# Optimization experiments

Measured on AMD Instinct MI355X. Metric: run time of the kernel, lower is better.

Reference implementation:

```python
import jax, jax.numpy as jnp
import numpy as np

D_MODEL = 1024
N_HEADS = 16
D_K = D_MODEL // N_HEADS
SCALE = float(np.sqrt(D_K))


def setup_inputs() -> dict:
    key = jax.random.key(0)
    ks = jax.random.split(key, 8)
    B, S = 2, 2048
    init = 1.0 / np.sqrt(D_MODEL)
    return {
        "query": jax.random.normal(ks[0], (B, S, D_MODEL), dtype=jnp.float32),
        "key": jax.random.normal(ks[1], (B, S, D_MODEL), dtype=jnp.float32),
        "value": jax.random.normal(ks[2], (B, S, D_MODEL), dtype=jnp.float32),
        "w_q": jax.random.uniform(ks[3], (D_MODEL, D_MODEL), jnp.float32, -init, init),
        "w_k": jax.random.uniform(ks[4], (D_MODEL, D_MODEL), jnp.float32, -init, init),
        "w_v": jax.random.uniform(ks[5], (D_MODEL, D_MODEL), jnp.float32, -init, init),
        "w_o": jax.random.uniform(ks[6], (D_MODEL, D_MODEL), jnp.float32, -init, init),
        "b_o": jax.random.uniform(ks[7], (D_MODEL,), jnp.float32, -init, init),
    }


def reference(query, key, value, w_q, w_k, w_v, w_o, b_o):
    B, S, _ = query.shape
    # nn.Linear computes x @ W.T; weights stored torch-style [out, in]
    def proj(x, w):
        # [B,S,D] -> [B,H,S,Dk]
        return (x @ w.T).reshape(B, S, N_HEADS, D_K).transpose(0, 2, 1, 3)

    Q = proj(query, w_q)
    K = proj(key, w_k)
    V = proj(value, w_v)
    scores = jnp.einsum("bhqd,bhkd->bhqk", Q, K) / SCALE  # [B,H,S,S]
    attn = jax.nn.softmax(scores, axis=-1)
    out = jnp.einsum("bhqk,bhkd->bhqd", attn, V)  # [B,H,S,Dk]
    out = out.transpose(0, 2, 1, 3).reshape(B, S, D_MODEL)
    out = out @ w_o.T + b_o
    return (out, attn)
```

## Files before the change

kernel.cpp:

```cpp
#include <hip/hip_runtime.h>
#include <hip/hip_bf16.h>

typedef unsigned int u32;
typedef unsigned short u16;
using bf16x8 = __attribute__((ext_vector_type(8))) short;
using f32x4  = __attribute__((ext_vector_type(4))) float;

#define S_LEN 2048
#define DK 64
#define NH 16
#define DMODEL 1024
#define NROWS 4096

__device__ __forceinline__ u16 f2bf(float f){
  u32 u = __builtin_bit_cast(u32, f);
  u += 0x7fffu + ((u >> 16) & 1u);
  return (u16)(u >> 16);
}

__device__ __forceinline__ void gload_lds16(const u16* g, u16* l){
  __builtin_amdgcn_global_load_lds(
      (__attribute__((address_space(1))) u32*)(void*)const_cast<u16*>(g),
      (__attribute__((address_space(3))) u32*)(void*)l, 16, 0, 0);
}

#define BARRIER_VM(N) do { \
  asm volatile("s_waitcnt vmcnt(" #N ") lgkmcnt(0)" ::: "memory"); \
  __builtin_amdgcn_s_barrier(); \
  __builtin_amdgcn_sched_barrier(0); \
} while (0)

__global__ void cvt_all(const float* __restrict__ q, const float* __restrict__ k,
                        const float* __restrict__ v, const float* __restrict__ wq,
                        const float* __restrict__ wk, const float* __restrict__ wv,
                        const float* __restrict__ wo, u16* __restrict__ ws)
{
  const int y = blockIdx.y;
  const int n4 = (y < 3) ? (NROWS*DMODEL/4) : (DMODEL*DMODEL/4);
  const int i = blockIdx.x * blockDim.x + threadIdx.x;
  if (i >= n4) return;
  const float* src = (y==0)?q:(y==1)?k:(y==2)?v:(y==3)?wq:(y==4)?wk:(y==5)?wv:wo;
  u16* dst = ws + ((y < 3) ? (size_t)y*(NROWS*DMODEL)
                           : (size_t)3*(NROWS*DMODEL) + (size_t)(y-3)*(DMODEL*DMODEL));
  float4 val = reinterpret_cast<const float4*>(src)[i];
  ushort4 o;
  o.x = f2bf(val.x); o.y = f2bf(val.y); o.z = f2bf(val.z); o.w = f2bf(val.w);
  reinterpret_cast<ushort4*>(dst)[i] = o;
}

template<bool OUTGEMM>
__global__ __launch_bounds__(256)
void gemm_mha(const u16* __restrict__ Abase, const u16* __restrict__ Bbase,
              u16* __restrict__ Qh, u16* __restrict__ Kh, u16* __restrict__ Vt,
              float* __restrict__ Out, const float* __restrict__ bias)
{
  __shared__ u16 smem[32768];
  u16* As = smem;
  u16* Bs = smem + 16384;

  const int tid  = threadIdx.x;
  const int lane = tid & 63;
  const int wid  = tid >> 6;
  const int lo = lane & 15, hi = lane >> 4;
  const int z = OUTGEMM ? 0 : blockIdx.z;
  const int m0 = blockIdx.x * 128;
  const int n0 = blockIdx.y * 128;
  const u16* ga = Abase + (size_t)z * (NROWS*DMODEL)  + (size_t)m0 * DMODEL;
  const u16* gb = Bbase + (size_t)z * (DMODEL*DMODEL) + (size_t)n0 * DMODEL;

  const int wm = (wid >> 1) * 64;
  const int wn = (wid & 1) * 64;

  f32x4 acc[4][4] = {};

  auto stage = [&](int buf, int kt){
    const u16* a = ga + kt * 64;
    const u16* b = gb + kt * 64;
    #pragma unroll
    for (int i = 0; i < 4; ++i){
      const int chunk = i*256 + tid;
      const int row = chunk >> 3, c8 = chunk & 7;
      gload_lds16(a + (size_t)row*DMODEL + c8*8, &As[buf*8192 + (i*256 + wid*64)*8]);
      gload_lds16(b + (size_t)row*DMODEL + c8*8, &Bs[buf*8192 + (i*256 + wid*64)*8]);
    }
  };

  stage(0, 0);
  __syncthreads();

  for (int t = 0; t < DMODEL/64; ++t){
    const int buf = t & 1;
    if (t + 1 < DMODEL/64) stage(buf ^ 1, t + 1);
    const u16* as = &As[buf*8192];
    const u16* bs = &Bs[buf*8192];
    #pragma unroll
    for (int ks = 0; ks < 2; ++ks){
      bf16x8 af[4], bfr[4];
      #pragma unroll
      for (int i = 0; i < 4; ++i){
        af[i]  = *reinterpret_cast<const bf16x8*>(&as[(wm + i*16 + lo)*64 + ks*32 + hi*8]);
        bfr[i] = *reinterpret_cast<const bf16x8*>(&bs[(wn + i*16 + lo)*64 + ks*32 + hi*8]);
      }
      #pragma unroll
      for (int mi = 0; mi < 4; ++mi)
        #pragma unroll
        for (int ni = 0; ni < 4; ++ni)
          acc[mi][ni] = __builtin_amdgcn_mfma_f32_16x16x32_bf16(af[mi], bfr[ni], acc[mi][ni], 0, 0, 0);
    }
    __syncthreads();
  }

  if constexpr (OUTGEMM){
    #pragma unroll
    for (int mi = 0; mi < 4; ++mi)
    #pragma unroll
    for (int ni = 0; ni < 4; ++ni)
    #pragma unroll
    for (int r = 0; r < 4; ++r){
      const int m = m0 + wm + mi*16 + hi*4 + r;
      const int n = n0 + wn + ni*16 + lo;
      __builtin_nontemporal_store(acc[mi][ni][r] + bias[n],
                                  &Out[(size_t)m * DMODEL + n]);
    }
  } else {
    const float scale = (z == 0) ? 0.18033688011112043f : 1.0f;
    if (z == 2){
      #pragma unroll
      for (int mi = 0; mi < 4; ++mi)
      #pragma unroll
      for (int ni = 0; ni < 4; ++ni)
      #pragma unroll
      for (int r = 0; r < 4; ++r)
        smem[(size_t)(wn + ni*16 + lo)*136 + wm + mi*16 + hi*4 + r] = f2bf(acc[mi][ni][r]);
    } else {
      #pragma unroll
      for (int mi = 0; mi < 4; ++mi)
      #pragma unroll
      for (int ni = 0; ni < 4; ++ni)
      #pragma unroll
      for (int r = 0; r < 4; ++r)
        smem[(size_t)(wm + mi*16 + hi*4 + r)*136 + wn + ni*16 + lo] = f2bf(acc[mi][ni][r] * scale);
    }
    __syncthreads();
    const int b = m0 >> 11, s0 = m0 & 2047;
    #pragma unroll
    for (int it = 0; it < 8; ++it){
      const int c = it*256 + tid;
      const int rr = c >> 4, cc = c & 15;
      bf16x8 v = *reinterpret_cast<const bf16x8*>(&smem[(size_t)rr*136 + cc*8]);
      if (z == 2){
        const int gn = n0 + rr, h = gn >> 6, d = gn & 63;
        *reinterpret_cast<bf16x8*>(&Vt[(((size_t)(b*NH + h))*DK + d)*S_LEN + s0 + cc*8]) = v;
      } else {
        const int gn = n0 + cc*8, h = gn >> 6, d0 = gn & 63;
        u16* dst = z ? Kh : Qh;
        *reinterpret_cast<bf16x8*>(&dst[(((size_t)(b*NH + h))*S_LEN + s0 + rr)*DK + d0]) = v;
      }
    }
  }
}

__global__ __launch_bounds__(512)
void attn_fused(const u16* __restrict__ Qh, const u16* __restrict__ Kh,
                const u16* __restrict__ Vt, float* __restrict__ attn,
                u16* __restrict__ ctx)
{
  constexpr int S = S_LEN;
  __shared__ u16 SM[26624];

  const int tid = threadIdx.x, lane = tid & 63, w = tid >> 6;
  const int lo = lane & 15, hi = lane >> 4;
  float* Pf = (float*)(SM + 16384);

  const int idx = blockIdx.x;
  const int slot = idx >> 3;
  const int qt = slot & 15;
  const int bh = (idx & 7) + 8 * (slot >> 4);

  const int q0 = qt*128 + w*16;
  const u16* Qb = Qh + (size_t)bh * S * DK;
  const u16* Kb = Kh + (size_t)bh * S * DK;
  const u16* Vb = Vt + (size_t)bh * DK * S;
  float* attn_b = attn + (size_t)bh * S * S;

  bf16x8 aq[2];
  #pragma unroll
  for (int ks = 0; ks < 2; ++ks)
    aq[ks] = *reinterpret_cast<const bf16x8*>(
        &Qb[(size_t)(q0 + lo) * DK + ks*32 + hi*8]);

  auto qk = [&](const u16* tile, f32x4 (&s)[4]){
    #pragma unroll
    for (int ks = 0; ks < 2; ++ks){
      bf16x8 bk[4];
      #pragma unroll
      for (int kf = 0; kf < 4; ++kf){
        const int row = kf*16 + lo;
        bk[kf] = *reinterpret_cast<const bf16x8*>(
            &tile[row*64 + (((ks*4 + hi) ^ (row&7))*8)]);
      }
      #pragma unroll
      for (int kf = 0; kf < 4; ++kf)
        s[kf] = __builtin_amdgcn_mfma_f32_16x16x32_bf16(aq[ks], bk[kf], s[kf], 0, 0, 0);
    }
  };

  auto stage128 = [&](u16* dst, int t16){
    const u16* kt = Kb + (size_t)t16 * 128 * DK;
    #pragma unroll
    for (int i = 0; i < 2; ++i){
      const int u_ = i*512 + tid;
      const int r = u_ >> 3, c = u_ & 7;
      gload_lds16(kt + (size_t)r*DK + ((c ^ (r&7))*8), dst + (i*512 + w*64)*8);
    }
  };
  auto p1buf = [&](int i){ return SM + (size_t)(i % 3) * 8192; };

  stage128(p1buf(0), 0);
  stage128(p1buf(1), 1);
  BARRIER_VM(2);
  float l_part[4] = {};
  for (int t = 0; t < S/128; ++t){
    if (t + 2 < S/128) stage128(p1buf(t + 2), t + 2);
    const u16* cur = p1buf(t);
    #pragma unroll
    for (int sub = 0; sub < 2; ++sub){
      f32x4 s[4] = {};
      qk(cur + sub*4096, s);
      #pragma unroll
      for (int r = 0; r < 4; ++r)
        l_part[r] += exp2f(s[0][r]) + exp2f(s[1][r]) + exp2f(s[2][r]) + exp2f(s[3][r]);
    }
    if (t < S/128 - 1){
      if (t < S/128 - 2) { BARRIER_VM(2); }
      else               { BARRIER_VM(0); }
    }
  }
  float inv_l[4];
  #pragma unroll
  for (int r = 0; r < 4; ++r){
    float v = l_part[r];
    v += __shfl_xor(v, 1, 64);
    v += __shfl_xor(v, 2, 64);
    v += __shfl_xor(v, 4, 64);
    v += __shfl_xor(v, 8, 64);
    inv_l[r] = 1.0f / v;
  }
  BARRIER_VM(0);

  const int sr = tid >> 3, sc = tid & 7;
  auto stageK = [&](int buf, int t){
    gload_lds16(Kb + (size_t)t*64*DK + (size_t)sr*DK + ((sc ^ (sr&7))*8),
                SM + buf*8192 + w*512);
  };
  auto stageV = [&](int buf, int t){
    gload_lds16(Vb + (size_t)sr*S + t*64 + ((sc ^ (sr&7))*8),
                SM + buf*8192 + 4096 + w*512);
  };

  stageK(0, 0); stageV(0, 0);
  BARRIER_VM(0);
  f32x4 o[4] = {};
  for (int t = 0; t < S/64; ++t){
    const int buf = t & 1;
    if (t + 1 < S/64){ stageK(buf ^ 1, t + 1); stageV(buf ^ 1, t + 1); }
    f32x4 s[4] = {};
    qk(SM + buf*8192, s);

    #pragma unroll
    for (int half = 0; half < 2; ++half){
      #pragma unroll
      for (int k2 = 0; k2 < 2; ++k2){
        const int kf = half*2 + k2;
        #pragma unroll
        for (int r = 0; r < 4; ++r){
          const int row = hi*4 + r;
          const int col = k2*16 + lo;
          Pf[w*640 + row*40 + ((((col>>2) ^ (row&7)) << 2) | (col & 3))] =
              exp2f(s[kf][r]) * inv_l[r];
        }
      }
      #pragma unroll
      for (int j = 0; j < 2; ++j){
        const int row = j*8 + (lane >> 3);
        const int cb  = (lane & 7) * 4;
        f32x4 vv = *reinterpret_cast<const f32x4*>(
            &Pf[w*640 + row*40 + ((((cb>>2) ^ (row&7)) << 2))]);
        __builtin_nontemporal_store(vv, reinterpret_cast<f32x4*>(
            &attn_b[(size_t)(q0 + row)*S + t*64 + half*32 + cb]));
      }
      {
        const int row = lo;
        const f32x4 pa = *reinterpret_cast<const f32x4*>(
            &Pf[w*640 + row*40 + (((2*hi) ^ (row&7)) << 2)]);
        const f32x4 pb = *reinterpret_cast<const f32x4*>(
            &Pf[w*640 + row*40 + (((2*hi + 1) ^ (row&7)) << 2)]);
        union { bf16x8 v; __hip_bfloat162 h[4]; } u_;
        u_.h[0] = __float22bfloat162_rn(float2{pa[0], pa[1]});
        u_.h[1] = __float22bfloat162_rn(float2{pa[2], pa[3]});
        u_.h[2] = __float22bfloat162_rn(float2{pb[0], pb[1]});
        u_.h[3] = __float22bfloat162_rn(float2{pb[2], pb[3]});
        bf16x8 bv[4];
        #pragma unroll
        for (int df = 0; df < 4; ++df){
          const int vrow = df*16 + lo;
          bv[df] = *reinterpret_cast<const bf16x8*>(
              &SM[buf*8192 + 4096 + vrow*64 + (((half*4 + hi) ^ (vrow&7))*8)]);
        }
        #pragma unroll
        for (int df = 0; df < 4; ++df)
          o[df] = __builtin_amdgcn_mfma_f32_16x16x32_bf16(u_.v, bv[df], o[df], 0, 0, 0);
      }
    }

    if (t + 1 < S/64){
      BARRIER_VM(4);
    }
  }

  {
    u16* Pw = (u16*)(Pf + (size_t)w * 640);
    #pragma unroll
    for (int df = 0; df < 4; ++df)
      #pragma unroll
      for (int r = 0; r < 4; ++r)
        Pw[(hi*4 + r)*64 + df*16 + lo] = f2bf(o[df][r]);
    const int b = bh >> 4, h = bh & 15;
    #pragma unroll
    for (int i = 0; i < 2; ++i){
      const int c = i*64 + lane;
      const int row = c >> 3, d0 = (c & 7) * 8;
      bf16x8 v = *reinterpret_cast<const bf16x8*>(&Pw[row*64 + d0]);
      *reinterpret_cast<bf16x8*>(
          &ctx[((size_t)b*S + q0 + row)*DMODEL + h*DK + d0]) = v;
    }
  }
}

extern "C" void kernel_launch(void* const* d_in, const int* in_sizes, int n_in,
                              void* d_out, int out_size, void* d_ws, size_t ws_size,
                              hipStream_t stream)
{
  const float* q_in = (const float*)d_in[0];
  const float* k_in = (const float*)d_in[1];
  const float* v_in = (const float*)d_in[2];
  const float* wq   = (const float*)d_in[3];
  const float* wk   = (const float*)d_in[4];
  const float* wv   = (const float*)d_in[5];
  const float* wo   = (const float*)d_in[6];
  const float* bo   = (const float*)d_in[7];

  u16* ws = (u16*)d_ws;
  u16* X  = ws;
  u16* W  = ws + (size_t)3*NROWS*DMODEL;
  u16* Wob= W  + (size_t)3*DMODEL*DMODEL;
  u16* Qh = W  + (size_t)4*DMODEL*DMODEL;
  u16* Kh = Qh + (size_t)NROWS*DMODEL;
  u16* Vt = Kh + (size_t)NROWS*DMODEL;
  u16* Ctx= Vt + (size_t)NROWS*DMODEL;

  cvt_all<<<dim3(4096, 7), 256, 0, stream>>>(q_in, k_in, v_in, wq, wk, wv, wo, ws);

  gemm_mha<false><<<dim3(32, 8, 3), 256, 0, stream>>>(X, W, Qh, Kh, Vt, nullptr, nullptr);

  float* out0 = (float*)d_out;
  float* attn = out0 + (size_t)NROWS * DMODEL;
  attn_fused<<<dim3(512), 512, 0, stream>>>(Qh, Kh, Vt, attn, Ctx);

  gemm_mha<true><<<dim3(32, 8), 256, 0, stream>>>(Ctx, Wob, nullptr, nullptr, nullptr, out0, bo);
}
```

Before: 221.6 us.

## Split output GEMM into narrower tiles and restructure attention staging

The templated GEMM is split into a QKV projection kernel and a separate output-projection kernel. The output kernel uses 128x64 tiles, doubling the block count to fill more compute units. The attention kernel's row-sum pass now uses double-buffered 256-row K tiles instead of a triple-buffered 128-row ring. The probability pass processes all 64 columns per step with a wider padded P scratch buffer, and context is written directly from registers rather than staged through LDS. These changes trade larger LDS use and uncoalesced scalar ctx stores for fewer barriers and better GEMM occupancy.

```diff
diff --git a/kernel.cpp b/kernel.cpp
--- a/kernel.cpp
+++ b/kernel.cpp
@@ -48,11 +48,9 @@
   reinterpret_cast<ushort4*>(dst)[i] = o;
 }
 
-template<bool OUTGEMM>
 __global__ __launch_bounds__(256)
-void gemm_mha(const u16* __restrict__ Abase, const u16* __restrict__ Bbase,
-              u16* __restrict__ Qh, u16* __restrict__ Kh, u16* __restrict__ Vt,
-              float* __restrict__ Out, const float* __restrict__ bias)
+void gemm_qkv(const u16* __restrict__ Abase, const u16* __restrict__ Bbase,
+              u16* __restrict__ Qh, u16* __restrict__ Kh, u16* __restrict__ Vt)
 {
   __shared__ u16 smem[32768];
   u16* As = smem;
@@ -62,7 +60,7 @@
   const int lane = tid & 63;
   const int wid  = tid >> 6;
   const int lo = lane & 15, hi = lane >> 4;
-  const int z = OUTGEMM ? 0 : blockIdx.z;
+  const int z = blockIdx.z;
   const int m0 = blockIdx.x * 128;
   const int n0 = blockIdx.y * 128;
   const u16* ga = Abase + (size_t)z * (NROWS*DMODEL)  + (size_t)m0 * DMODEL;
@@ -110,53 +108,117 @@
     __syncthreads();
   }
 
-  if constexpr (OUTGEMM){
+  const float scale = (z == 0) ? 0.18033688011112043f : 1.0f;
+  if (z == 2){
     #pragma unroll
     for (int mi = 0; mi < 4; ++mi)
     #pragma unroll
     for (int ni = 0; ni < 4; ++ni)
     #pragma unroll
-    for (int r = 0; r < 4; ++r){
-      const int m = m0 + wm + mi*16 + hi*4 + r;
-      const int n = n0 + wn + ni*16 + lo;
-      __builtin_nontemporal_store(acc[mi][ni][r] + bias[n],
-                                  &Out[(size_t)m * DMODEL + n]);
-    }
+    for (int r = 0; r < 4; ++r)
+      smem[(size_t)(wn + ni*16 + lo)*136 + wm + mi*16 + hi*4 + r] = f2bf(acc[mi][ni][r]);
   } else {
-    const float scale = (z == 0) ? 0.18033688011112043f : 1.0f;
+    #pragma unroll
+    for (int mi = 0; mi < 4; ++mi)
+    #pragma unroll
+    for (int ni = 0; ni < 4; ++ni)
+    #pragma unroll
+    for (int r = 0; r < 4; ++r)
+      smem[(size_t)(wm + mi*16 + hi*4 + r)*136 + wn + ni*16 + lo] = f2bf(acc[mi][ni][r] * scale);
+  }
+  __syncthreads();
+  const int b = m0 >> 11, s0 = m0 & 2047;
+  #pragma unroll
+  for (int it = 0; it < 8; ++it){
+    const int c = it*256 + tid;
+    const int rr = c >> 4, cc = c & 15;
+    bf16x8 v = *reinterpret_cast<const bf16x8*>(&smem[(size_t)rr*136 + cc*8]);
     if (z == 2){
+      const int gn = n0 + rr, h = gn >> 6, d = gn & 63;
+      *reinterpret_cast<bf16x8*>(&Vt[(((size_t)(b*NH + h))*DK + d)*S_LEN + s0 + cc*8]) = v;
+    } else {
+      const int gn = n0 + cc*8, h = gn >> 6, d0 = gn & 63;
+      u16* dst = z ? Kh : Qh;
+      *reinterpret_cast<bf16x8*>(&dst[(((size_t)(b*NH + h))*S_LEN + s0 + rr)*DK + d0]) = v;
+    }
+  }
+}
+
+__global__ __launch_bounds__(256)
+void gemm_out(const u16* __restrict__ Abase, const u16* __restrict__ Bbase,
+              float* __restrict__ Out, const float* __restrict__ bias)
+{
+  __shared__ u16 smem[24576];
+  u16* As = smem;
+  u16* Bs = smem + 16384;
+
+  const int tid  = threadIdx.x;
+  const int lane = tid & 63;
+  const int wid  = tid >> 6;
+  const int lo = lane & 15, hi = lane >> 4;
+  const int m0 = blockIdx.x * 128;
+  const int n0 = blockIdx.y * 64;
+  const u16* ga = Abase + (size_t)m0 * DMODEL;
+  const u16* gb = Bbase + (size_t)n0 * DMODEL;
+
+  const int wm = (wid >> 1) * 64;
+  const int wn = (wid & 1) * 32;
+
+  f32x4 acc[4][2] = {};
+
+  auto stage = [&](int buf, int kt){
+    const u16* a = ga + kt * 64;
+    const u16* b = gb + kt * 64;
+    #pragma unroll
+    for (int i = 0; i < 4; ++i){
+      const int chunk = i*256 + tid;
+      const int row = chunk >> 3, c8 = chunk & 7;
+      gload_lds16(a + (size_t)row*DMODEL + c8*8, &As[buf*8192 + (i*256 + wid*64)*8]);
+    }
+    #pragma unroll
+    for (int i = 0; i < 2; ++i){
+      const int chunk = i*256 + tid;
+      const int row = chunk >> 3, c8 = chunk & 7;
+      gload_lds16(b + (size_t)row*DMODEL + c8*8, &Bs[buf*4096 + (i*256 + wid*64)*8]);
+    }
+  };
+
+  stage(0, 0);
+  __syncthreads();
+
+  for (int t = 0; t < DMODEL/64; ++t){
+    const int buf = t & 1;
+    if (t + 1 < DMODEL/64) stage(buf ^ 1, t + 1);
+    const u16* as = &As[buf*8192];
+    const u16* bs = &Bs[buf*4096];
+    #pragma unroll
+    for (int ks = 0; ks < 2; ++ks){
+      bf16x8 af[4], bfr[2];
+      #pragma unroll
+      for (int i = 0; i < 4; ++i)
+        af[i]  = *reinterpret_cast<const bf16x8*>(&as[(wm + i*16 + lo)*64 + ks*32 + hi*8]);
+      #pragma unroll
+      for (int i = 0; i < 2; ++i)
+        bfr[i] = *reinterpret_cast<const bf16x8*>(&bs[(wn + i*16 + lo)*64 + ks*32 + hi*8]);
       #pragma unroll
       for (int mi = 0; mi < 4; ++mi)
-      #pragma unroll
-      for (int ni = 0; ni < 4; ++ni)
-      #pragma unroll
-      for (int r = 0; r < 4; ++r)
-        smem[(size_t)(wn + ni*16 + lo)*136 + wm + mi*16 + hi*4 + r] = f2bf(acc[mi][ni][r]);
-    } else {
-      #pragma unroll
-      for (int mi = 0; mi < 4; ++mi)
-      #pragma unroll
-      for (int ni = 0; ni < 4; ++ni)
-      #pragma unroll
-      for (int r = 0; r < 4; ++r)
-        smem[(size_t)(wm + mi*16 + hi*4 + r)*136 + wn + ni*16 + lo] = f2bf(acc[mi][ni][r] * scale);
+        #pragma unroll
+        for (int ni = 0; ni < 2; ++ni)
+          acc[mi][ni] = __builtin_amdgcn_mfma_f32_16x16x32_bf16(af[mi], bfr[ni], acc[mi][ni], 0, 0, 0);
     }
     __syncthreads();
-    const int b = m0 >> 11, s0 = m0 & 2047;
-    #pragma unroll
-    for (int it = 0; it < 8; ++it){
-      const int c = it*256 + tid;
-      const int rr = c >> 4, cc = c & 15;
-      bf16x8 v = *reinterpret_cast<const bf16x8*>(&smem[(size_t)rr*136 + cc*8]);
-      if (z == 2){
-        const int gn = n0 + rr, h = gn >> 6, d = gn & 63;
-        *reinterpret_cast<bf16x8*>(&Vt[(((size_t)(b*NH + h))*DK + d)*S_LEN + s0 + cc*8]) = v;
-      } else {
-        const int gn = n0 + cc*8, h = gn >> 6, d0 = gn & 63;
-        u16* dst = z ? Kh : Qh;
-        *reinterpret_cast<bf16x8*>(&dst[(((size_t)(b*NH + h))*S_LEN + s0 + rr)*DK + d0]) = v;
-      }
-    }
+  }
+
+  #pragma unroll
+  for (int mi = 0; mi < 4; ++mi)
+  #pragma unroll
+  for (int ni = 0; ni < 2; ++ni)
+  #pragma unroll
+  for (int r = 0; r < 4; ++r){
+    const int m = m0 + wm + mi*16 + hi*4 + r;
+    const int n = n0 + wn + ni*16 + lo;
+    __builtin_nontemporal_store(acc[mi][ni][r] + bias[n],
+                                &Out[(size_t)m * DMODEL + n]);
   }
 }
 
@@ -166,11 +228,11 @@
                 u16* __restrict__ ctx)
 {
   constexpr int S = S_LEN;
-  __shared__ u16 SM[26624];
+  __shared__ u16 SM[34816];
+  float* Pf = (float*)(SM + 16384);
 
   const int tid = threadIdx.x, lane = tid & 63, w = tid >> 6;
   const int lo = lane & 15, hi = lane >> 4;
-  float* Pf = (float*)(SM + 16384);
 
   const int idx = blockIdx.x;
   const int slot = idx >> 3;
@@ -205,96 +267,91 @@
     }
   };
 
-  auto stage128 = [&](u16* dst, int t16){
-    const u16* kt = Kb + (size_t)t16 * 128 * DK;
-    #pragma unroll
-    for (int i = 0; i < 2; ++i){
-      const int u_ = i*512 + tid;
-      const int r = u_ >> 3, c = u_ & 7;
-      gload_lds16(kt + (size_t)r*DK + ((c ^ (r&7))*8), dst + (i*512 + w*64)*8);
-    }
-  };
-  auto p1buf = [&](int i){ return SM + (size_t)(i % 3) * 8192; };
-
-  stage128(p1buf(0), 0);
-  stage128(p1buf(1), 1);
-  BARRIER_VM(2);
-  float l_part[4] = {};
-  for (int t = 0; t < S/128; ++t){
-    if (t + 2 < S/128) stage128(p1buf(t + 2), t + 2);
-    const u16* cur = p1buf(t);
-    #pragma unroll
-    for (int sub = 0; sub < 2; ++sub){
+  {
+    u16* b0 = SM;
+    u16* b1 = SM + 16384;
+    auto stage256 = [&](u16* dst, int t8){
+      const u16* kt = Kb + (size_t)t8 * 256 * DK;
+      #pragma unroll
+      for (int i = 0; i < 4; ++i){
+        const int u_ = i*512 + tid;
+        const int r = u_ >> 3, c = u_ & 7;
+        gload_lds16(kt + (size_t)r*DK + ((c ^ (r&7))*8), dst + (i*512 + w*64)*8);
+      }
+    };
+    stage256(b0, 0);
+    __syncthreads();
+    float l_part[4] = {};
+    for (int t = 0; t < S/256; ++t){
+      u16* cur = (t & 1) ? b1 : b0;
+      if (t + 1 < S/256) stage256((t & 1) ? b0 : b1, t + 1);
+      #pragma unroll
+      for (int sub = 0; sub < 4; ++sub){
+        f32x4 s[4] = {};
+        qk(cur + sub*4096, s);
+        #pragma unroll
+        for (int r = 0; r < 4; ++r)
+          l_part[r] += exp2f(s[0][r]) + exp2f(s[1][r]) + exp2f(s[2][r]) + exp2f(s[3][r]);
+      }
+      if (t < S/256 - 1) __syncthreads();
+    }
+    float inv_l[4];
+    #pragma unroll
+    for (int r = 0; r < 4; ++r){
+      float v = l_part[r];
+      v += __shfl_xor(v, 1, 64);
+      v += __shfl_xor(v, 2, 64);
+      v += __shfl_xor(v, 4, 64);
+      v += __shfl_xor(v, 8, 64);
+      inv_l[r] = 1.0f / v;
+    }
+
+    const int sr = tid >> 3, sc = tid & 7;
+    auto stageK = [&](int buf, int t){
+      gload_lds16(Kb + (size_t)t*64*DK + (size_t)sr*DK + ((sc ^ (sr&7))*8),
+                  SM + buf*8192 + w*512);
+    };
+    auto stageV = [&](int buf, int t){
+      gload_lds16(Vb + (size_t)sr*S + t*64 + ((sc ^ (sr&7))*8),
+                  SM + buf*8192 + 4096 + w*512);
+    };
+
+    stageK(0, 0); stageV(0, 0);
+    BARRIER_VM(0);
+    f32x4 o[4] = {};
+    float* Pw = Pf + (size_t)w * 1152;
+    for (int t = 0; t < S/64; ++t){
+      const int buf = t & 1;
+      if (t + 1 < S/64){ stageK(buf ^ 1, t + 1); stageV(buf ^ 1, t + 1); }
       f32x4 s[4] = {};
-      qk(cur + sub*4096, s);
-      #pragma unroll
-      for (int r = 0; r < 4; ++r)
-        l_part[r] += exp2f(s[0][r]) + exp2f(s[1][r]) + exp2f(s[2][r]) + exp2f(s[3][r]);
-    }
-    if (t < S/128 - 1){
-      if (t < S/128 - 2) { BARRIER_VM(2); }
-      else               { BARRIER_VM(0); }
-    }
-  }
-  float inv_l[4];
-  #pragma unroll
-  for (int r = 0; r < 4; ++r){
-    float v = l_part[r];
-    v += __shfl_xor(v, 1, 64);
-    v += __shfl_xor(v, 2, 64);
-    v += __shfl_xor(v, 4, 64);
-    v += __shfl_xor(v, 8, 64);
-    inv_l[r] = 1.0f / v;
-  }
-  BARRIER_VM(0);
-
-  const int sr = tid >> 3, sc = tid & 7;
-  auto stageK = [&](int buf, int t){
-    gload_lds16(Kb + (size_t)t*64*DK + (size_t)sr*DK + ((sc ^ (sr&7))*8),
-                SM + buf*8192 + w*512);
-  };
-  auto stageV = [&](int buf, int t){
-    gload_lds16(Vb + (size_t)sr*S + t*64 + ((sc ^ (sr&7))*8),
-                SM + buf*8192 + 4096 + w*512);
-  };
-
-  stageK(0, 0); stageV(0, 0);
-  BARRIER_VM(0);
-  f32x4 o[4] = {};
-  for (int t = 0; t < S/64; ++t){
-    const int buf = t & 1;
-    if (t + 1 < S/64){ stageK(buf ^ 1, t + 1); stageV(buf ^ 1, t + 1); }
-    f32x4 s[4] = {};
-    qk(SM + buf*8192, s);
-
-    #pragma unroll
-    for (int half = 0; half < 2; ++half){
-      #pragma unroll
-      for (int k2 = 0; k2 < 2; ++k2){
-        const int kf = half*2 + k2;
+      qk(SM + buf*8192, s);
+
+      #pragma unroll
+      for (int kf = 0; kf < 4; ++kf)
         #pragma unroll
         for (int r = 0; r < 4; ++r){
           const int row = hi*4 + r;
-          const int col = k2*16 + lo;
-          Pf[w*640 + row*40 + ((((col>>2) ^ (row&7)) << 2) | (col & 3))] =
+          const int col = kf*16 + lo;
+          const int ch  = col >> 2;
+          Pw[row*72 + (((ch ^ (row&7)) << 2) | (col & 3))] =
               exp2f(s[kf][r]) * inv_l[r];
         }
-      }
-      #pragma unroll
-      for (int j = 0; j < 2; ++j){
-        const int row = j*8 + (lane >> 3);
-        const int cb  = (lane & 7) * 4;
+      #pragma unroll
+      for (int j = 0; j < 4; ++j){
+        const int row = j*4 + hi;
+        const int ch  = lo;
         f32x4 vv = *reinterpret_cast<const f32x4*>(
-            &Pf[w*640 + row*40 + ((((cb>>2) ^ (row&7)) << 2))]);
+            &Pw[row*72 + (((ch ^ (row&7)) << 2))]);
         __builtin_nontemporal_store(vv, reinterpret_cast<f32x4*>(
-            &attn_b[(size_t)(q0 + row)*S + t*64 + half*32 + cb]));
-      }
-      {
+            &attn_b[(size_t)(q0 + row)*S + t*64 + ch*4]));
+      }
+      #pragma unroll
+      for (int ks = 0; ks < 2; ++ks){
         const int row = lo;
-        const f32x4 pa = *reinterpret_cast<const f32x4*>(
-            &Pf[w*640 + row*40 + (((2*hi) ^ (row&7)) << 2)]);
-        const f32x4 pb = *reinterpret_cast<const f32x4*>(
-            &Pf[w*640 + row*40 + (((2*hi + 1) ^ (row&7)) << 2)]);
+        const int c0 = (2*(ks*4 + hi))     ^ (row&7);
+        const int c1 = (2*(ks*4 + hi) + 1) ^ (row&7);
+        const f32x4 pa = *reinterpret_cast<const f32x4*>(&Pw[row*72 + (c0 << 2)]);
+        const f32x4 pb = *reinterpret_cast<const f32x4*>(&Pw[row*72 + (c1 << 2)]);
         union { bf16x8 v; __hip_bfloat162 h[4]; } u_;
         u_.h[0] = __float22bfloat162_rn(float2{pa[0], pa[1]});
         u_.h[1] = __float22bfloat162_rn(float2{pa[2], pa[3]});
@@ -305,34 +362,26 @@
         for (int df = 0; df < 4; ++df){
           const int vrow = df*16 + lo;
           bv[df] = *reinterpret_cast<const bf16x8*>(
-              &SM[buf*8192 + 4096 + vrow*64 + (((half*4 + hi) ^ (vrow&7))*8)]);
+              &SM[buf*8192 + 4096 + vrow*64 + (((ks*4 + hi) ^ (vrow&7))*8)]);
         }
         #pragma unroll
         for (int df = 0; df < 4; ++df)
           o[df] = __builtin_amdgcn_mfma_f32_16x16x32_bf16(u_.v, bv[df], o[df], 0, 0, 0);
       }
-    }
-
-    if (t + 1 < S/64){
-      BARRIER_VM(4);
-    }
-  }
-
-  {
-    u16* Pw = (u16*)(Pf + (size_t)w * 640);
+
+      if (t + 1 < S/64){
+        BARRIER_VM(4);
+      }
+    }
+
+    const int b = bh >> 4, h = bh & 15;
     #pragma unroll
     for (int df = 0; df < 4; ++df)
-      #pragma unroll
-      for (int r = 0; r < 4; ++r)
-        Pw[(hi*4 + r)*64 + df*16 + lo] = f2bf(o[df][r]);
-    const int b = bh >> 4, h = bh & 15;
-    #pragma unroll
-    for (int i = 0; i < 2; ++i){
-      const int c = i*64 + lane;
-      const int row = c >> 3, d0 = (c & 7) * 8;
-      bf16x8 v = *reinterpret_cast<const bf16x8*>(&Pw[row*64 + d0]);
-      *reinterpret_cast<bf16x8*>(
-          &ctx[((size_t)b*S + q0 + row)*DMODEL + h*DK + d0]) = v;
+    #pragma unroll
+    for (int r = 0; r < 4; ++r){
+      const int qq = q0 + hi*4 + r;
+      const int d  = df*16 + lo;
+      ctx[((size_t)b * S + qq) * DMODEL + h*DK + d] = f2bf(o[df][r]);
     }
   }
 }
@@ -361,11 +410,11 @@
 
   cvt_all<<<dim3(4096, 7), 256, 0, stream>>>(q_in, k_in, v_in, wq, wk, wv, wo, ws);
 
-  gemm_mha<false><<<dim3(32, 8, 3), 256, 0, stream>>>(X, W, Qh, Kh, Vt, nullptr, nullptr);
+  gemm_qkv<<<dim3(32, 8, 3), 256, 0, stream>>>(X, W, Qh, Kh, Vt);
 
   float* out0 = (float*)d_out;
   float* attn = out0 + (size_t)NROWS * DMODEL;
   attn_fused<<<dim3(512), 512, 0, stream>>>(Qh, Kh, Vt, attn, Ctx);
 
-  gemm_mha<true><<<dim3(32, 8), 256, 0, stream>>>(Ctx, Wob, nullptr, nullptr, nullptr, out0, bo);
-}
+  gemm_out<<<dim3(32, 16), 256, 0, stream>>>(Ctx, Wob, out0, bo);
+}
```

After: 222.9 us. About the same (+0.6%).
